# Kernel tuning notes

Hardware: AMD Instinct MI355X
Metric: run time of the kernel (lower is better)

The kernel has to match this reference:

```python
import jax, jax.numpy as jnp
import numpy as np

NEG_SLOPE = 0.2  # PyG GATConv default leaky_relu slope


def gat_conv(x, ei, W, a_src, a_dst, b, heads, ch):
    """One PyG-style GATConv (eval mode, add_self_loops already applied to ei)."""
    N = x.shape[0]
    h = (x @ W).reshape(N, heads, ch)                      # [N,H,C]
    src, dst = ei[0], ei[1]
    al_s = jnp.sum(h * a_src, axis=-1)                     # [N,H]
    al_d = jnp.sum(h * a_dst, axis=-1)                     # [N,H]
    e = jax.nn.leaky_relu(al_s[src] + al_d[dst], NEG_SLOPE)  # [E,H]
    m = jax.ops.segment_max(e, dst, num_segments=N)        # stable softmax over in-edges
    ex = jnp.exp(e - m[dst])
    den = jax.ops.segment_sum(ex, dst, num_segments=N)
    alpha = ex / den[dst]                                  # [E,H]
    msg = alpha[:, :, None] * h[src]                       # [E,H,C]
    out = jax.ops.segment_sum(msg, dst, num_segments=N)    # [N,H,C]
    return out.reshape(N, heads * ch) + b


def setup_inputs() -> dict:
    key = jax.random.key(0)
    ks = jax.random.split(key, 12)
    N, E, D_in, C, H, D_out = 10000, 320000, 256, 128, 4, 64
    HC = H * C

    def glorot(k, shape):
        fan = shape[0] + shape[-1]
        return jax.random.normal(k, shape, dtype=jnp.float32) * np.sqrt(2.0 / fan)

    x = jax.random.normal(ks[0], (N, D_in), dtype=jnp.float32)
    edge_index = jax.random.randint(ks[1], (2, E), 0, N, dtype=jnp.int64)
    return {
        "x": x,
        "edge_index": edge_index,
        "W1": glorot(ks[2], (D_in, HC)),
        "a_src1": glorot(ks[3], (H, C)),
        "a_dst1": glorot(ks[4], (H, C)),
        "b1": jnp.zeros((HC,), dtype=jnp.float32),
        "W2": glorot(ks[5], (HC, HC)),
        "a_src2": glorot(ks[6], (H, C)),
        "a_dst2": glorot(ks[7], (H, C)),
        "b2": jnp.zeros((HC,), dtype=jnp.float32),
        "W3": glorot(ks[8], (HC, D_out)),
        "a_src3": glorot(ks[9], (1, D_out)),
        "a_dst3": glorot(ks[10], (1, D_out)),
        "b3": jnp.zeros((D_out,), dtype=jnp.float32),
    }


def reference(x, edge_index, W1, a_src1, a_dst1, b1, W2, a_src2, a_dst2, b2,
              W3, a_src3, a_dst3, b3):
    N = x.shape[0]
    loops = jnp.arange(N, dtype=edge_index.dtype)
    ei = jnp.concatenate([edge_index, jnp.stack([loops, loops])], axis=1)
    H, C = a_src1.shape
    h = jax.nn.elu(gat_conv(x, ei, W1, a_src1, a_dst1, b1, H, C))
    h = jax.nn.elu(gat_conv(h, ei, W2, a_src2, a_dst2, b2, H, C))
    out = gat_conv(h, ei, W3, a_src3, a_dst3, b3, 1, a_src3.shape[1])
    return out
```

## Files before the change

### kernel.cpp

```cpp
#include <hip/hip_runtime.h>

typedef short bf16x8 __attribute__((ext_vector_type(8)));
typedef float f32x4 __attribute__((ext_vector_type(4)));

__device__ __forceinline__ unsigned short f2bf(float f) {
    unsigned u = __float_as_uint(f);
    unsigned r = (u + 0x7fffu + ((u >> 16) & 1u)) >> 16;
    return (unsigned short)r;
}
__device__ __forceinline__ float bf2f(unsigned short u) {
    return __uint_as_float(((unsigned)u) << 16);
}

__device__ __forceinline__ void gload_lds16(const void* g, void* l) {
    __builtin_amdgcn_global_load_lds(
        (const __attribute__((address_space(1))) unsigned int*)g,
        (__attribute__((address_space(3))) unsigned int*)l, 16, 0, 0);
}

__global__ void k_prep(const float* __restrict__ W1, unsigned short* __restrict__ W1T,
                       const float* __restrict__ W2, unsigned short* __restrict__ W2T,
                       const float* __restrict__ W3, unsigned short* __restrict__ W3T,
                       const float* __restrict__ x, unsigned short* __restrict__ xb,
                       int* __restrict__ csr, int Mcap,
                       const int* __restrict__ ei, int E, int* __restrict__ deg,
                       int DIN, int HC, int DOUT, int N)
{
    int i = blockIdx.x * blockDim.x + threadIdx.x;
    int n1 = DIN * HC;
    int n2 = n1 + HC * HC;
    int n3 = n2 + HC * DOUT;
    int n4 = n3 + N * DIN;
    int n5 = n4 + Mcap;
    int n6 = n5 + E;
    if (i < n1) {
        int k = i / HC, n = i - k * HC;
        W1T[n * DIN + k] = f2bf(W1[i]);
    } else if (i < n2) {
        int j = i - n1;
        int k = j / HC, n = j - k * HC;
        W2T[n * HC + k] = f2bf(W2[j]);
    } else if (i < n3) {
        int j = i - n2;
        int k = j / DOUT, n = j - k * DOUT;
        W3T[n * HC + k] = f2bf(W3[j]);
    } else if (i < n4) {
        int j = i - n3;
        xb[j] = f2bf(x[j]);
    } else if (i < n5) {
        csr[i - n4] = -1;
    } else if (i < n6) {
        atomicAdd(&deg[ei[E + (i - n5)]], 1);
    }
}

__global__ void k_scan(const int* __restrict__ deg, int* __restrict__ off,
                       int* __restrict__ cur, int N) {
    __shared__ int sums[1024];
    int t = threadIdx.x;
    int chunk = (N + 1023) >> 10;
    int lo = t * chunk;
    int hi = lo + chunk; if (hi > N) hi = N;
    if (lo > N) lo = N;
    int s = 0;
    for (int i = lo; i < hi; ++i) s += (deg[i] + 4) & ~3;
    sums[t] = s;
    __syncthreads();
    for (int dd = 1; dd < 1024; dd <<= 1) {
        int v = (t >= dd) ? sums[t - dd] : 0;
        __syncthreads();
        sums[t] += v;
        __syncthreads();
    }
    int run = sums[t] - s;
    for (int i = lo; i < hi; ++i) { off[i] = run; cur[i] = run; run += (deg[i] + 4) & ~3; }
    if (t == 1023) off[N] = run;
}
__global__ void k_fill(const int* __restrict__ ei, int E, int N,
                       int* cur, int* __restrict__ csr, int* __restrict__ dstarr) {
    int i = blockIdx.x * blockDim.x + threadIdx.x;
    if (i < E) {
        int s = ei[i], d = ei[E + i];
        int pos = atomicAdd(&cur[d], 1);
        csr[pos] = s;
        dstarr[pos] = d;
    } else if (i < E + N) {
        int nn = i - E;
        int pos = atomicAdd(&cur[nn], 1);
        csr[pos] = nn;
        dstarr[pos] = nn;
    }
}

template <bool OUTBF>
__global__ __launch_bounds__(256) void k_gemm(
    const unsigned short* __restrict__ A, const unsigned short* __restrict__ BT,
    void* __restrict__ D, int M, int K, int Nc, int tiles_n)
{
    int wid = blockIdx.x * (blockDim.x >> 6) + (threadIdx.x >> 6);
    int tiles_m = (M + 63) >> 6;
    if (wid >= tiles_m * tiles_n) return;
    int lane = threadIdx.x & 63;
    int tm = wid / tiles_n, tn = wid - tm * tiles_n;
    int m0 = tm << 6, n0 = tn << 6;
    int r = lane & 15, q = lane >> 4;

    const unsigned short* Arow[4];
    const unsigned short* Brow[4];
#pragma unroll
    for (int i = 0; i < 4; ++i) {
        int row = m0 + 16 * i + r; row = row < M ? row : M - 1;
        Arow[i] = A + (size_t)row * K + q * 8;
        Brow[i] = BT + (size_t)(n0 + 16 * i + r) * K + q * 8;
    }

    f32x4 acc[4][4] = {};
    bf16x8 a[4], b[4], a2[4], b2[4];
#pragma unroll
    for (int i = 0; i < 4; ++i) {
        a[i] = *(const bf16x8*)(Arow[i]);
        b[i] = *(const bf16x8*)(Brow[i]);
    }
    for (int k0 = 0; k0 < K; k0 += 32) {
        int kn = k0 + 32;
        if (kn < K) {
#pragma unroll
            for (int i = 0; i < 4; ++i) {
                a2[i] = *(const bf16x8*)(Arow[i] + kn);
                b2[i] = *(const bf16x8*)(Brow[i] + kn);
            }
        }
#pragma unroll
        for (int i = 0; i < 4; ++i)
#pragma unroll
            for (int j = 0; j < 4; ++j)
                acc[i][j] = __builtin_amdgcn_mfma_f32_16x16x32_bf16(a[i], b[j], acc[i][j], 0, 0, 0);
        if (kn < K) {
#pragma unroll
            for (int i = 0; i < 4; ++i) { a[i] = a2[i]; b[i] = b2[i]; }
        }
    }
#pragma unroll
    for (int i = 0; i < 4; ++i) {
        int rowb = m0 + 16 * i + q * 4;
#pragma unroll
        for (int rr = 0; rr < 4; ++rr) {
            int row = rowb + rr;
            if (row < M) {
#pragma unroll
                for (int j = 0; j < 4; ++j) {
                    int col = n0 + 16 * j + r;
                    if (OUTBF)
                        ((unsigned short*)D)[(size_t)row * Nc + col] = f2bf(acc[i][j][rr]);
                    else
                        ((float*)D)[(size_t)row * Nc + col] = acc[i][j][rr];
                }
            }
        }
    }
}

__global__ __launch_bounds__(256) void k_gemm_lds(
    const unsigned short* __restrict__ A, const unsigned short* __restrict__ BT,
    unsigned short* __restrict__ D, int M, int K, int Nc, int tiles_n)
{
    __shared__ unsigned short As[128 * 32];
    __shared__ unsigned short Bs[64 * 32];
    int tm = blockIdx.x / tiles_n, tn = blockIdx.x - tm * tiles_n;
    int m0 = tm << 7, n0 = tn << 6;
    int tid = threadIdx.x;
    int w = tid >> 6, lane = tid & 63;
    int wr = w >> 1, wc = w & 1;
    int r = lane & 15, q = lane >> 4;

    int lrow = lane >> 2;
    int lch = (lane & 3) * 8;
    int ga0 = m0 + w * 16 + lrow;       if (ga0 >= M) ga0 = M - 1;
    int ga1 = m0 + (w + 4) * 16 + lrow; if (ga1 >= M) ga1 = M - 1;
    const unsigned short* pa0 = A + (size_t)ga0 * K + lch;
    const unsigned short* pa1 = A + (size_t)ga1 * K + lch;
    const unsigned short* pb  = BT + (size_t)(n0 + w * 16 + lrow) * K + lch;
    unsigned short* lA0 = As + w * 512;
    unsigned short* lA1 = As + (w + 4) * 512;
    unsigned short* lB  = Bs + w * 512;

    const unsigned short* arp = As + (wr * 64 + r) * 32 + q * 8;
    const unsigned short* brp = Bs + (wc * 32 + r) * 32 + q * 8;

    f32x4 acc[4][2] = {};
    for (int k0 = 0; k0 < K; k0 += 32) {
        gload_lds16(pa0 + k0, lA0);
        gload_lds16(pa1 + k0, lA1);
        gload_lds16(pb + k0, lB);
        __syncthreads();
        bf16x8 a[4], b[2];
#pragma unroll
        for (int i = 0; i < 4; ++i) a[i] = *(const bf16x8*)(arp + i * 16 * 32);
#pragma unroll
        for (int j = 0; j < 2; ++j) b[j] = *(const bf16x8*)(brp + j * 16 * 32);
#pragma unroll
        for (int i = 0; i < 4; ++i)
#pragma unroll
            for (int j = 0; j < 2; ++j)
                acc[i][j] = __builtin_amdgcn_mfma_f32_16x16x32_bf16(a[i], b[j], acc[i][j], 0, 0, 0);
        __syncthreads();
    }
#pragma unroll
    for (int i = 0; i < 4; ++i) {
        int rowb = m0 + wr * 64 + 16 * i + q * 4;
#pragma unroll
        for (int rr = 0; rr < 4; ++rr) {
            int row = rowb + rr;
            if (row < M) {
#pragma unroll
                for (int j = 0; j < 2; ++j) {
                    int col = n0 + wc * 32 + 16 * j + r;
                    D[(size_t)row * Nc + col] = f2bf(acc[i][j][rr]);
                }
            }
        }
    }
}

template <int HCt, int Ht>
__global__ __launch_bounds__(256) void k_al(
    const unsigned short* __restrict__ h, const float* __restrict__ asrc,
    const float* __restrict__ adst,
    float* __restrict__ als, float* __restrict__ ald, int N)
{
    int wid = blockIdx.x * (blockDim.x >> 6) + (threadIdx.x >> 6);
    if (wid >= N) return;
    int lane = threadIdx.x & 63;
    const int CH = HCt / 64;
    const int Gs = 64 / Ht;
    float s = 0.f, d = 0.f;
    if constexpr (CH == 8) {
        const uint4* hr = (const uint4*)(h + (size_t)wid * HCt) + lane;
        uint4 hv = *hr;
        unsigned wds[4] = {hv.x, hv.y, hv.z, hv.w};
        const f32x4* as4 = (const f32x4*)(asrc + lane * 8);
        const f32x4* ad4 = (const f32x4*)(adst + lane * 8);
        f32x4 av0 = as4[0], av1 = as4[1], dv0 = ad4[0], dv1 = ad4[1];
        float hf[8];
#pragma unroll
        for (int wv = 0; wv < 4; ++wv) {
            hf[2 * wv]     = __uint_as_float(wds[wv] << 16);
            hf[2 * wv + 1] = __uint_as_float(wds[wv] & 0xffff0000u);
        }
#pragma unroll
        for (int j = 0; j < 4; ++j) {
            s += hf[j] * av0[j] + hf[4 + j] * av1[j];
            d += hf[j] * dv0[j] + hf[4 + j] * dv1[j];
        }
    } else {
        float hv = bf2f(h[(size_t)wid * HCt + lane]);
        s = hv * asrc[lane];
        d = hv * adst[lane];
    }
#pragma unroll
    for (int dd = 1; dd < Gs; dd <<= 1) {
        s += __shfl_xor(s, dd);
        d += __shfl_xor(d, dd);
    }
    if ((lane & (Gs - 1)) == 0) {
        int hh = lane / Gs;
        als[wid * Ht + hh] = s;
        ald[wid * Ht + hh] = d;
    }
}

__global__ void k_alpha4(const float* __restrict__ als, const float* __restrict__ ald,
                         const int* __restrict__ csr, const int* __restrict__ dstarr,
                         const int* __restrict__ off, int N,
                         float* __restrict__ alpha, int Mcap)
{
    int t = blockIdx.x * blockDim.x + threadIdx.x;
    if (t >= off[N]) return;
    int s = csr[t];
    if (s < 0) {
#pragma unroll
        for (int h = 0; h < 4; ++h) alpha[(size_t)h * Mcap + t] = 0.f;
        return;
    }
    int d = dstarr[t];
    f32x4 a = *(const f32x4*)(als + (size_t)s * 4);
    f32x4 b = *(const f32x4*)(ald + (size_t)d * 4);
#pragma unroll
    for (int h = 0; h < 4; ++h) {
        float l = a[h] + b[h];
        l = l > 0.f ? l : 0.2f * l;
        alpha[(size_t)h * Mcap + t] = __expf(l);
    }
}

template <bool DOELU>
__global__ __launch_bounds__(256) void k_aggr4b(
    const unsigned short* __restrict__ h, const float* __restrict__ alpha,
    const int* __restrict__ off, const int* __restrict__ csr,
    const float* __restrict__ bias,
    unsigned short* __restrict__ outp, int N, int nodeBlocks, int Mcap)
{
    int head = blockIdx.x / nodeBlocks;
    int nb = blockIdx.x - head * nodeBlocks;
    int n = nb * 4 + (threadIdx.x >> 6);
    if (n >= N) return;
    int lane = threadIdx.x & 63;
    int g = lane >> 4;
    int p = lane & 15;
    int q0 = (off[n] >> 2) + g, q1 = off[n + 1] >> 2;

    float acc[8] = {};
    float den = 0.f;
    const unsigned short* hbase = h + head * 128 + p * 8;
    const int4* csr4 = (const int4*)csr;
    const f32x4* al4 = (const f32x4*)(alpha + (size_t)head * Mcap);

    auto fmaq = [&](float a, const uint4& hq) {
        unsigned wds[4] = {hq.x, hq.y, hq.z, hq.w};
#pragma unroll
        for (int wv = 0; wv < 4; ++wv) {
            acc[2 * wv]     += a * __uint_as_float(wds[wv] << 16);
            acc[2 * wv + 1] += a * __uint_as_float(wds[wv] & 0xffff0000u);
        }
    };

    for (int q = q0; q < q1; q += 4) {
        int4 cs = csr4[q];
        f32x4 av = al4[q];
        int c0 = cs.x < 0 ? 0 : cs.x;
        int c1 = cs.y < 0 ? 0 : cs.y;
        int c2 = cs.z < 0 ? 0 : cs.z;
        int c3 = cs.w < 0 ? 0 : cs.w;
        uint4 h0 = *(const uint4*)(hbase + ((size_t)(unsigned)c0 << 9));
        uint4 h1 = *(const uint4*)(hbase + ((size_t)(unsigned)c1 << 9));
        uint4 h2 = *(const uint4*)(hbase + ((size_t)(unsigned)c2 << 9));
        uint4 h3 = *(const uint4*)(hbase + ((size_t)(unsigned)c3 << 9));
        den += (av[0] + av[1]) + (av[2] + av[3]);
        fmaq(av[0], h0);
        fmaq(av[1], h1);
        fmaq(av[2], h2);
        fmaq(av[3], h3);
    }

    den += __shfl_xor(den, 16);
    den += __shfl_xor(den, 32);
#pragma unroll
    for (int j = 0; j < 8; ++j) {
        acc[j] += __shfl_xor(acc[j], 16);
        acc[j] += __shfl_xor(acc[j], 32);
    }

    if (g == 0) {
        float inv = 1.f / den;
        int cb = head * 128 + p * 8;
        unsigned ww[4];
#pragma unroll
        for (int wv = 0; wv < 4; ++wv) {
            float v0 = acc[2 * wv] * inv + bias[cb + 2 * wv];
            float v1 = acc[2 * wv + 1] * inv + bias[cb + 2 * wv + 1];
            if (DOELU) {
                v0 = v0 > 0.f ? v0 : expm1f(v0);
                v1 = v1 > 0.f ? v1 : expm1f(v1);
            }
            ww[wv] = (unsigned)f2bf(v0) | ((unsigned)f2bf(v1) << 16);
        }
        uint4 o; o.x = ww[0]; o.y = ww[1]; o.z = ww[2]; o.w = ww[3];
        *((uint4*)(outp + (size_t)n * 512 + cb)) = o;
    }
}

__global__ __launch_bounds__(256) void k_aggr1b(
    const unsigned short* __restrict__ h, const float* __restrict__ als,
    const float* __restrict__ aldv, const int* __restrict__ off,
    const int* __restrict__ csr, const float* __restrict__ bias,
    float* __restrict__ outp, int N)
{
    int n = blockIdx.x * (blockDim.x >> 6) + (threadIdx.x >> 6);
    if (n >= N) return;
    int lane = threadIdx.x & 63;
    int g = lane >> 4;
    int p = lane & 15;
    int q0 = (off[n] >> 2) + g, q1 = off[n + 1] >> 2;
    float aldh = aldv[n];

    float acc[4] = {};
    float den = 0.f;
    const unsigned short* hbase = h + p * 4;
    const int4* csr4 = (const int4*)csr;

    auto aof = [&](int ss) -> float {
        int sc = ss < 0 ? 0 : ss;
        float l = als[sc] + aldh;
        l = l > 0.f ? l : 0.2f * l;
        float e = __expf(l);
        return ss < 0 ? 0.f : e;
    };
    auto fmaq = [&](float a, const uint2& hq) {
        den += a;
        acc[0] += a * __uint_as_float(hq.x << 16);
        acc[1] += a * __uint_as_float(hq.x & 0xffff0000u);
        acc[2] += a * __uint_as_float(hq.y << 16);
        acc[3] += a * __uint_as_float(hq.y & 0xffff0000u);
    };

    for (int q = q0; q < q1; q += 4) {
        int4 cs = csr4[q];
        float a0 = aof(cs.x), a1 = aof(cs.y), a2 = aof(cs.z), a3 = aof(cs.w);
        uint2 h0 = *(const uint2*)(hbase + ((size_t)(unsigned)(cs.x < 0 ? 0 : cs.x) << 6));
        uint2 h1 = *(const uint2*)(hbase + ((size_t)(unsigned)(cs.y < 0 ? 0 : cs.y) << 6));
        uint2 h2 = *(const uint2*)(hbase + ((size_t)(unsigned)(cs.z < 0 ? 0 : cs.z) << 6));
        uint2 h3 = *(const uint2*)(hbase + ((size_t)(unsigned)(cs.w < 0 ? 0 : cs.w) << 6));
        fmaq(a0, h0);
        fmaq(a1, h1);
        fmaq(a2, h2);
        fmaq(a3, h3);
    }

    den += __shfl_xor(den, 16);
    den += __shfl_xor(den, 32);
#pragma unroll
    for (int j = 0; j < 4; ++j) {
        acc[j] += __shfl_xor(acc[j], 16);
        acc[j] += __shfl_xor(acc[j], 32);
    }
    if (g == 0) {
        float inv = 1.f / den;
        f32x4 o;
#pragma unroll
        for (int j = 0; j < 4; ++j)
            o[j] = acc[j] * inv + bias[p * 4 + j];
        *((f32x4*)(outp + (size_t)n * 64 + p * 4)) = o;
    }
}

extern "C" void kernel_launch(void* const* d_in, const int* in_sizes, int n_in,
                              void* d_out, int out_size, void* d_ws, size_t ws_size,
                              hipStream_t stream)
{
    const float* x   = (const float*)d_in[0];
    const int*   ei  = (const int*)d_in[1];
    const float* W1  = (const float*)d_in[2];
    const float* as1 = (const float*)d_in[3];
    const float* ad1 = (const float*)d_in[4];
    const float* b1  = (const float*)d_in[5];
    const float* W2  = (const float*)d_in[6];
    const float* as2 = (const float*)d_in[7];
    const float* ad2 = (const float*)d_in[8];
    const float* b2  = (const float*)d_in[9];
    const float* W3  = (const float*)d_in[10];
    const float* as3 = (const float*)d_in[11];
    const float* ad3 = (const float*)d_in[12];
    const float* b3  = (const float*)d_in[13];

    const int DIN = 256, HC = 512, DOUT = 64;
    int N = in_sizes[0] / DIN;
    int E = in_sizes[1] / 2;
    int Mcap = E + 4 * N;

    char* w = (char*)d_ws;
    auto alloc = [&](size_t bytes) -> char* {
        char* p = w;
        w += (bytes + 255) & ~(size_t)255;
        return p;
    };
    int* deg    = (int*)alloc((size_t)N * 4);
    int* cur    = (int*)alloc((size_t)N * 4);
    int* off    = (int*)alloc((size_t)(N + 1) * 4);
    int* csr    = (int*)alloc((size_t)Mcap * 4);
    int* dstarr = (int*)alloc((size_t)Mcap * 4);
    unsigned short* W1T = (unsigned short*)alloc((size_t)HC * DIN * 2);
    unsigned short* W2T = (unsigned short*)alloc((size_t)HC * HC * 2);
    unsigned short* W3T = (unsigned short*)alloc((size_t)DOUT * HC * 2);
    unsigned short* xb  = (unsigned short*)alloc((size_t)N * DIN * 2);
    unsigned short* act = (unsigned short*)alloc((size_t)N * HC * 2);
    unsigned short* hb  = (unsigned short*)alloc((size_t)N * HC * 2);
    unsigned short* hb3 = (unsigned short*)alloc((size_t)N * DOUT * 2);
    float* als   = (float*)alloc((size_t)N * 4 * 4);
    float* ald   = (float*)alloc((size_t)N * 4 * 4);
    float* alpha = (float*)alloc((size_t)Mcap * 4 * 4);

    hipMemsetAsync(deg, 0, (size_t)N * 4, stream);
    int prep_total = DIN * HC + HC * HC + HC * DOUT + N * DIN + Mcap + E;
    k_prep<<<(prep_total + 255) / 256, 256, 0, stream>>>(
        W1, W1T, W2, W2T, W3, W3T, x, xb, csr, Mcap, ei, E, deg, DIN, HC, DOUT, N);
    k_scan<<<1, 1024, 0, stream>>>(deg, off, cur, N);
    k_fill<<<(E + N + 255) / 256, 256, 0, stream>>>(ei, E, N, cur, csr, dstarr);

    int tiles_m = (N + 63) / 64;
    auto gemm_blocks = [&](int tn) { return (tiles_m * tn + 3) / 4; };
    int tm128 = (N + 127) / 128;
    int nwave_blocks = (N + 3) / 4;
    int nodeBlocks = (N + 3) / 4;
    int alpha_blocks = (Mcap + 255) / 256;

    k_gemm_lds<<<tm128 * (HC / 64), 256, 0, stream>>>(xb, W1T, hb, N, DIN, HC, HC / 64);
    k_al<512, 4><<<nwave_blocks, 256, 0, stream>>>(hb, as1, ad1, als, ald, N);
    k_alpha4<<<alpha_blocks, 256, 0, stream>>>(als, ald, csr, dstarr, off, N, alpha, Mcap);
    k_aggr4b<true><<<4 * nodeBlocks, 256, 0, stream>>>(hb, alpha, off, csr, b1, act, N, nodeBlocks, Mcap);

    k_gemm_lds<<<tm128 * (HC / 64), 256, 0, stream>>>(act, W2T, hb, N, HC, HC, HC / 64);
    k_al<512, 4><<<nwave_blocks, 256, 0, stream>>>(hb, as2, ad2, als, ald, N);
    k_alpha4<<<alpha_blocks, 256, 0, stream>>>(als, ald, csr, dstarr, off, N, alpha, Mcap);
    k_aggr4b<true><<<4 * nodeBlocks, 256, 0, stream>>>(hb, alpha, off, csr, b2, act, N, nodeBlocks, Mcap);

    k_gemm<true><<<gemm_blocks(1), 256, 0, stream>>>(act, W3T, hb3, N, HC, DOUT, 1);
    k_al<64, 1><<<nwave_blocks, 256, 0, stream>>>(hb3, as3, ad3, als, ald, N);
    k_aggr1b<<<nwave_blocks, 256, 0, stream>>>(hb3, als, ald, off, csr, b3, (float*)d_out, N);
}
```

Measured before the change: 289.2 us.

## Fuse edge attention into aggregation and attention-logit dot into final GEMM

Removes the separate per-edge alpha kernel and its alpha and dstarr buffers. The aggregation kernel now computes leaky-relu and exp on the fly from the per-node logits, so it no longer writes and re-reads a large per-edge alpha array. The layer-3 GEMM also computes the source and destination attention dot products from its accumulators through shuffles, which drops the separate k_al launch. In exchange, each of the four head blocks recomputes exp for every edge and makes a scattered read of als per edge.

```diff
diff --git a/kernel.cpp b/kernel.cpp
--- a/kernel.cpp
+++ b/kernel.cpp
@@ -77,25 +77,25 @@
     if (t == 1023) off[N] = run;
 }
 __global__ void k_fill(const int* __restrict__ ei, int E, int N,
-                       int* cur, int* __restrict__ csr, int* __restrict__ dstarr) {
+                       int* cur, int* __restrict__ csr) {
     int i = blockIdx.x * blockDim.x + threadIdx.x;
     if (i < E) {
         int s = ei[i], d = ei[E + i];
         int pos = atomicAdd(&cur[d], 1);
         csr[pos] = s;
-        dstarr[pos] = d;
     } else if (i < E + N) {
         int nn = i - E;
         int pos = atomicAdd(&cur[nn], 1);
         csr[pos] = nn;
-        dstarr[pos] = nn;
-    }
-}
-
-template <bool OUTBF>
+    }
+}
+
+template <bool OUTBF, bool DOAL>
 __global__ __launch_bounds__(256) void k_gemm(
     const unsigned short* __restrict__ A, const unsigned short* __restrict__ BT,
-    void* __restrict__ D, int M, int K, int Nc, int tiles_n)
+    void* __restrict__ D, int M, int K, int Nc, int tiles_n,
+    const float* __restrict__ asrc, const float* __restrict__ adst,
+    float* __restrict__ als, float* __restrict__ ald)
 {
     int wid = blockIdx.x * (blockDim.x >> 6) + (threadIdx.x >> 6);
     int tiles_m = (M + 63) >> 6;
@@ -155,6 +155,30 @@
                     else
                         ((float*)D)[(size_t)row * Nc + col] = acc[i][j][rr];
                 }
+            }
+        }
+    }
+    if (DOAL) {
+        float asl[4], adl[4];
+#pragma unroll
+        for (int j = 0; j < 4; ++j) { asl[j] = asrc[16 * j + r]; adl[j] = adst[16 * j + r]; }
+#pragma unroll
+        for (int i = 0; i < 4; ++i) {
+#pragma unroll
+            for (int rr = 0; rr < 4; ++rr) {
+                float s = 0.f, d = 0.f;
+#pragma unroll
+                for (int j = 0; j < 4; ++j) {
+                    s += acc[i][j][rr] * asl[j];
+                    d += acc[i][j][rr] * adl[j];
+                }
+#pragma unroll
+                for (int dd = 1; dd < 16; dd <<= 1) {
+                    s += __shfl_xor(s, dd);
+                    d += __shfl_xor(d, dd);
+                }
+                int row = m0 + 16 * i + q * 4 + rr;
+                if (r == 0 && row < M) { als[row] = s; ald[row] = d; }
             }
         }
     }
@@ -269,36 +293,13 @@
     }
 }
 
-__global__ void k_alpha4(const float* __restrict__ als, const float* __restrict__ ald,
-                         const int* __restrict__ csr, const int* __restrict__ dstarr,
-                         const int* __restrict__ off, int N,
-                         float* __restrict__ alpha, int Mcap)
-{
-    int t = blockIdx.x * blockDim.x + threadIdx.x;
-    if (t >= off[N]) return;
-    int s = csr[t];
-    if (s < 0) {
-#pragma unroll
-        for (int h = 0; h < 4; ++h) alpha[(size_t)h * Mcap + t] = 0.f;
-        return;
-    }
-    int d = dstarr[t];
-    f32x4 a = *(const f32x4*)(als + (size_t)s * 4);
-    f32x4 b = *(const f32x4*)(ald + (size_t)d * 4);
-#pragma unroll
-    for (int h = 0; h < 4; ++h) {
-        float l = a[h] + b[h];
-        l = l > 0.f ? l : 0.2f * l;
-        alpha[(size_t)h * Mcap + t] = __expf(l);
-    }
-}
-
 template <bool DOELU>
-__global__ __launch_bounds__(256) void k_aggr4b(
-    const unsigned short* __restrict__ h, const float* __restrict__ alpha,
+__global__ __launch_bounds__(256) void k_aggr4c(
+    const unsigned short* __restrict__ h, const float* __restrict__ als,
+    const float* __restrict__ ald,
     const int* __restrict__ off, const int* __restrict__ csr,
     const float* __restrict__ bias,
-    unsigned short* __restrict__ outp, int N, int nodeBlocks, int Mcap)
+    unsigned short* __restrict__ outp, int N, int nodeBlocks)
 {
     int head = blockIdx.x / nodeBlocks;
     int nb = blockIdx.x - head * nodeBlocks;
@@ -308,13 +309,20 @@
     int g = lane >> 4;
     int p = lane & 15;
     int q0 = (off[n] >> 2) + g, q1 = off[n + 1] >> 2;
+    float aldh = ald[n * 4 + head];
 
     float acc[8] = {};
     float den = 0.f;
     const unsigned short* hbase = h + head * 128 + p * 8;
     const int4* csr4 = (const int4*)csr;
-    const f32x4* al4 = (const f32x4*)(alpha + (size_t)head * Mcap);
-
+
+    auto aof = [&](int ss) -> float {
+        int sc = ss < 0 ? 0 : ss;
+        float l = als[sc * 4 + head] + aldh;
+        l = l > 0.f ? l : 0.2f * l;
+        float e = __expf(l);
+        return ss < 0 ? 0.f : e;
+    };
     auto fmaq = [&](float a, const uint4& hq) {
         unsigned wds[4] = {hq.x, hq.y, hq.z, hq.w};
 #pragma unroll
@@ -326,7 +334,6 @@
 
     for (int q = q0; q < q1; q += 4) {
         int4 cs = csr4[q];
-        f32x4 av = al4[q];
         int c0 = cs.x < 0 ? 0 : cs.x;
         int c1 = cs.y < 0 ? 0 : cs.y;
         int c2 = cs.z < 0 ? 0 : cs.z;
@@ -335,11 +342,12 @@
         uint4 h1 = *(const uint4*)(hbase + ((size_t)(unsigned)c1 << 9));
         uint4 h2 = *(const uint4*)(hbase + ((size_t)(unsigned)c2 << 9));
         uint4 h3 = *(const uint4*)(hbase + ((size_t)(unsigned)c3 << 9));
-        den += (av[0] + av[1]) + (av[2] + av[3]);
-        fmaq(av[0], h0);
-        fmaq(av[1], h1);
-        fmaq(av[2], h2);
-        fmaq(av[3], h3);
+        float a0 = aof(cs.x), a1 = aof(cs.y), a2 = aof(cs.z), a3 = aof(cs.w);
+        den += (a0 + a1) + (a2 + a3);
+        fmaq(a0, h0);
+        fmaq(a1, h1);
+        fmaq(a2, h2);
+        fmaq(a3, h3);
     }
 
     den += __shfl_xor(den, 16);
@@ -467,7 +475,6 @@
     int* cur    = (int*)alloc((size_t)N * 4);
     int* off    = (int*)alloc((size_t)(N + 1) * 4);
     int* csr    = (int*)alloc((size_t)Mcap * 4);
-    int* dstarr = (int*)alloc((size_t)Mcap * 4);
     unsigned short* W1T = (unsigned short*)alloc((size_t)HC * DIN * 2);
     unsigned short* W2T = (unsigned short*)alloc((size_t)HC * HC * 2);
     unsigned short* W3T = (unsigned short*)alloc((size_t)DOUT * HC * 2);
@@ -477,33 +484,29 @@
     unsigned short* hb3 = (unsigned short*)alloc((size_t)N * DOUT * 2);
     float* als   = (float*)alloc((size_t)N * 4 * 4);
     float* ald   = (float*)alloc((size_t)N * 4 * 4);
-    float* alpha = (float*)alloc((size_t)Mcap * 4 * 4);
 
     hipMemsetAsync(deg, 0, (size_t)N * 4, stream);
     int prep_total = DIN * HC + HC * HC + HC * DOUT + N * DIN + Mcap + E;
     k_prep<<<(prep_total + 255) / 256, 256, 0, stream>>>(
         W1, W1T, W2, W2T, W3, W3T, x, xb, csr, Mcap, ei, E, deg, DIN, HC, DOUT, N);
     k_scan<<<1, 1024, 0, stream>>>(deg, off, cur, N);
-    k_fill<<<(E + N + 255) / 256, 256, 0, stream>>>(ei, E, N, cur, csr, dstarr);
+    k_fill<<<(E + N + 255) / 256, 256, 0, stream>>>(ei, E, N, cur, csr);
 
     int tiles_m = (N + 63) / 64;
     auto gemm_blocks = [&](int tn) { return (tiles_m * tn + 3) / 4; };
     int tm128 = (N + 127) / 128;
     int nwave_blocks = (N + 3) / 4;
     int nodeBlocks = (N + 3) / 4;
-    int alpha_blocks = (Mcap + 255) / 256;
 
     k_gemm_lds<<<tm128 * (HC / 64), 256, 0, stream>>>(xb, W1T, hb, N, DIN, HC, HC / 64);
     k_al<512, 4><<<nwave_blocks, 256, 0, stream>>>(hb, as1, ad1, als, ald, N);
-    k_alpha4<<<alpha_blocks, 256, 0, stream>>>(als, ald, csr, dstarr, off, N, alpha, Mcap);
-    k_aggr4b<true><<<4 * nodeBlocks, 256, 0, stream>>>(hb, alpha, off, csr, b1, act, N, nodeBlocks, Mcap);
+    k_aggr4c<true><<<4 * nodeBlocks, 256, 0, stream>>>(hb, als, ald, off, csr, b1, act, N, nodeBlocks);
 
     k_gemm_lds<<<tm128 * (HC / 64), 256, 0, stream>>>(act, W2T, hb, N, HC, HC, HC / 64);
     k_al<512, 4><<<nwave_blocks, 256, 0, stream>>>(hb, as2, ad2, als, ald, N);
-    k_alpha4<<<alpha_blocks, 256, 0, stream>>>(als, ald, csr, dstarr, off, N, alpha, Mcap);
-    k_aggr4b<true><<<4 * nodeBlocks, 256, 0, stream>>>(hb, alpha, off, csr, b2, act, N, nodeBlocks, Mcap);
-
-    k_gemm<true><<<gemm_blocks(1), 256, 0, stream>>>(act, W3T, hb3, N, HC, DOUT, 1);
-    k_al<64, 1><<<nwave_blocks, 256, 0, stream>>>(hb3, as3, ad3, als, ald, N);
+    k_aggr4c<true><<<4 * nodeBlocks, 256, 0, stream>>>(hb, als, ald, off, csr, b2, act, N, nodeBlocks);
+
+    k_gemm<true, true><<<gemm_blocks(1), 256, 0, stream>>>(
+        act, W3T, hb3, N, HC, DOUT, 1, as3, ad3, als, ald);
     k_aggr1b<<<nwave_blocks, 256, 0, stream>>>(hb3, als, ald, off, csr, b3, (float*)d_out, N);
 }
```

New measurement: 301.6 us. 4.3% more time.
